# Optimization experiments

Hardware: AMD Instinct MI355X
Metric: run time of the kernel (lower is better)

Reference implementation:

```python
import math
import jax, jax.numpy as jnp
import numpy as np

B, L, D, HID, DFF, EA, NH = 16, 511, 1024, 512, 2048, 256, 4
S = L + 1  # tgt length = bos + L; also memory length (max_basis_dim+1)


def _pe(seq, d):
    pos = jnp.arange(seq, dtype=jnp.float32)[:, None]
    div = jnp.exp(jnp.arange(0, d, 2, dtype=jnp.float32) * (-math.log(10000.0) / d))
    pe = jnp.zeros((seq, d), jnp.float32)
    return pe.at[:, 0::2].set(jnp.sin(pos * div)).at[:, 1::2].set(jnp.cos(pos * div))


def _ln(x, w, b):
    m = x.mean(-1, keepdims=True)
    v = ((x - m) ** 2).mean(-1, keepdims=True)
    return (x - m) / jnp.sqrt(v + 1e-5) * w + b


def _leaky(x):
    return jnp.where(x >= 0, x, 0.01 * x)


def _mha(xq, xkv, qkv_w, qkv_b, out_w, out_b, mask):
    d = xq.shape[-1]
    hd = d // NH
    wq, wk, wv = jnp.split(qkv_w, 3, axis=0)
    bq, bk, bv = jnp.split(qkv_b, 3)
    q = (xq @ wq.T + bq).reshape(xq.shape[0], xq.shape[1], NH, hd)
    k = (xkv @ wk.T + bk).reshape(xkv.shape[0], xkv.shape[1], NH, hd)
    v = (xkv @ wv.T + bv).reshape(xkv.shape[0], xkv.shape[1], NH, hd)
    att = jnp.einsum('bqhd,bkhd->bhqk', q, k) / math.sqrt(hd)
    if mask is not None:
        att = att + mask
    p = jax.nn.softmax(att, axis=-1)
    o = jnp.einsum('bhqk,bkhd->bqhd', p, v).reshape(xq.shape[0], xq.shape[1], d)
    return o @ out_w.T + out_b


def setup_inputs() -> dict:
    key = jax.random.key(0)
    ks = iter(jax.random.split(key, 40))
    rn = lambda shape, s=0.02: jax.random.normal(next(ks), shape, jnp.float32) * s
    return dict(
        gs_norms_embedding=jax.random.normal(next(ks), (B, S, HID), jnp.float32),
        prev_action_embedding=jax.random.normal(next(ks), (B, EA), jnp.float32),
        current_action_embedding=jax.random.normal(next(ks), (B, EA), jnp.float32),
        target_gs_norms=jax.random.normal(next(ks), (B, L), jnp.float32),
        bos=rn((1, 1), 1.0),
        inp_w1=rn((HID, 1)), inp_b1=rn((HID,)),
        inp_w2=rn((HID, HID)), inp_b2=rn((HID,)),
        sa_qkv_w=rn((3, 3 * D, D)), sa_qkv_b=rn((3, 3 * D)),
        sa_out_w=rn((3, D, D)), sa_out_b=rn((3, D)),
        ca_qkv_w=rn((3, 3 * D, D)), ca_qkv_b=rn((3, 3 * D)),
        ca_out_w=rn((3, D, D)), ca_out_b=rn((3, D)),
        ln_w=jnp.ones((3, 3, D), jnp.float32), ln_b=jnp.zeros((3, 3, D), jnp.float32),
        ff_w1=rn((3, DFF, D)), ff_b1=rn((3, DFF)),
        ff_w2=rn((3, D, DFF)), ff_b2=rn((3, D)),
        proj_w1=rn((HID, D)), proj_b1=rn((HID,)),
        proj_w2=rn((1, HID)), proj_b2=rn((1,)),
        basis_dim=jax.random.randint(next(ks), (B,), 0, S),
    )


def reference(gs_norms_embedding, prev_action_embedding, current_action_embedding,
              target_gs_norms, bos, inp_w1, inp_b1, inp_w2, inp_b2,
              sa_qkv_w, sa_qkv_b, sa_out_w, sa_out_b,
              ca_qkv_w, ca_qkv_b, ca_out_w, ca_out_b,
              ln_w, ln_b, ff_w1, ff_b1, ff_w2, ff_b2,
              proj_w1, proj_b1, proj_w2, proj_b2, basis_dim):
    b = gs_norms_embedding.shape[0]
    prev = jnp.broadcast_to(prev_action_embedding[:, None, :], (b, S, EA))
    cur = jnp.broadcast_to(current_action_embedding[:, None, :], (b, S, EA))
    # teacher-forced target: [bos, target] -> input_projection -> pos enc
    tgt_scalar = jnp.concatenate([jnp.broadcast_to(bos, (b, 1)), target_gs_norms], axis=1)  # [B,S]
    x = _leaky(tgt_scalar[..., None] @ inp_w1.T + inp_b1) @ inp_w2.T + inp_b2  # [B,S,HID]
    x = x + _pe(S, HID)
    tgt = jnp.concatenate([x, prev, cur], axis=-1)  # [B,S,D]
    mem = jnp.concatenate([gs_norms_embedding, prev, cur], axis=-1)  # [B,S,D]
    mask = jnp.triu(jnp.full((S, S), -1e9, jnp.float32), k=1)
    h = tgt
    for l in range(3):  # post-norm TransformerDecoderLayer, activation=relu
        h = _ln(h + _mha(h, h, sa_qkv_w[l], sa_qkv_b[l], sa_out_w[l], sa_out_b[l], mask), ln_w[l, 0], ln_b[l, 0])
        h = _ln(h + _mha(h, mem, ca_qkv_w[l], ca_qkv_b[l], ca_out_w[l], ca_out_b[l], None), ln_w[l, 1], ln_b[l, 1])
        ff = jax.nn.relu(h @ ff_w1[l].T + ff_b1[l]) @ ff_w2[l].T + ff_b2[l]
        h = _ln(h + ff, ln_w[l, 2], ln_b[l, 2])
    out = (_leaky(h[:, 1:, :] @ proj_w1.T + proj_b1) @ proj_w2.T + proj_b2)[..., 0]  # [B,L]
    keep = jnp.arange(L)[None, :] < basis_dim[:, None]
    return jnp.where(keep, out, 0.0)
```

## Files before the change

kernel.cpp:

```cpp
#include <hip/hip_runtime.h>

typedef unsigned short u16;
typedef __attribute__((ext_vector_type(8))) short bf16x8;
typedef __attribute__((ext_vector_type(4))) float f32x4;

#define BB   16
#define LL   511
#define SS   512
#define DD   1024
#define HIDD 512
#define DFFF 2048
#define NHH  4
#define HDD  256
#define MTOK (BB*SS)

__device__ __forceinline__ float b2f(u16 u){ return __uint_as_float(((unsigned)u)<<16); }
__device__ __forceinline__ u16 f2b(float f){
    unsigned x = __float_as_uint(f);
    return (u16)((x + 0x7fffu + ((x>>16)&1u)) >> 16);
}
__device__ __forceinline__ float ldin(const void* p, size_t i, int f){
    return f ? ((const float*)p)[i] : b2f(((const u16*)p)[i]);
}
__device__ __forceinline__ void gload_lds16(const void* g, void* l){
    __builtin_amdgcn_global_load_lds((const __attribute__((address_space(1))) unsigned*)g,
                                     (__attribute__((address_space(3))) unsigned*)l, 16, 0, 0);
}

__global__ void detect_kernel(const u16* __restrict__ lnw, int* __restrict__ flag){
    if (threadIdx.x == 0 && blockIdx.x == 0) flag[0] = (lnw[0] == 0x3F80) ? 0 : 1;
}

__global__ void wconv_kernel(const void* __restrict__ w, size_t woff,
                             const void* __restrict__ b, size_t boff,
                             u16* __restrict__ dw, u16* __restrict__ db,
                             int nw, int nb, const int* __restrict__ flag){
    const int f = flag[0];
    const int idx = blockIdx.x*256 + threadIdx.x;
    const int stride = gridDim.x * 256;
    if (f){
        const float* wf = (const float*)w + woff;
        const float* bf = (const float*)b + boff;
        for (int i = idx*4; i < nw; i += stride*4){
            const float4 v = *(const float4*)&wf[i];
            ushort4 o; o.x=f2b(v.x); o.y=f2b(v.y); o.z=f2b(v.z); o.w=f2b(v.w);
            *(ushort4*)&dw[i] = o;
        }
        for (int i = idx*4; i < nb; i += stride*4){
            const float4 v = *(const float4*)&bf[i];
            ushort4 o; o.x=f2b(v.x); o.y=f2b(v.y); o.z=f2b(v.z); o.w=f2b(v.w);
            *(ushort4*)&db[i] = o;
        }
    } else {
        const u16* wu = (const u16*)w + woff;
        const u16* bu = (const u16*)b + boff;
        for (int i = idx*4; i < nw; i += stride*4) *(ushort4*)&dw[i] = *(const ushort4*)&wu[i];
        for (int i = idx*4; i < nb; i += stride*4) *(ushort4*)&db[i] = *(const ushort4*)&bu[i];
    }
}

__global__ void pe_kernel(float* __restrict__ pe){
    const int i = blockIdx.x*256 + threadIdx.x;
    const int s = i >> 9, c = i & 511;
    const float div = expf(-(float)(c & ~1) * (logf(10000.0f)/512.0f));
    const float ang = (float)s * div;
    pe[i] = (c & 1) ? cosf(ang) : sinf(ang);
}

__global__ void inp_u_kernel(const void* __restrict__ bos, const void* __restrict__ target,
                             const void* __restrict__ w1, const void* __restrict__ b1,
                             u16* __restrict__ U, const int* __restrict__ flag){
    const int f = flag[0];
    const int i = blockIdx.x*256 + threadIdx.x;
    const int m = i >> 9, c = i & 511;
    const int b = m >> 9, s = m & 511;
    const float ts = (s == 0) ? ldin(bos, 0, f) : ldin(target, b*LL + s - 1, f);
    float v = ts * ldin(w1, c, f) + ldin(b1, c, f);
    U[i] = f2b(v >= 0.f ? v : 0.01f*v);
}

__global__ void concat_kernel(const void* __restrict__ gs, const void* __restrict__ prev,
                              const void* __restrict__ cur, u16* __restrict__ tgt,
                              u16* __restrict__ mem, const int* __restrict__ flag){
    const int f = flag[0];
    const int i = blockIdx.x*256 + threadIdx.x;
    const int m = i >> 10, c = i & 1023;
    if (c < 512){
        mem[i] = f2b(ldin(gs, (size_t)m*512 + c, f));
    } else {
        const float pc = (c < 768) ? ldin(prev, (m>>9)*256 + (c-512), f)
                                   : ldin(cur,  (m>>9)*256 + (c-768), f);
        const u16 pb = f2b(pc);
        tgt[i] = pb; mem[i] = pb;
    }
}

template<int ACT, int RES>
__device__ __forceinline__ void gemm_body(const u16* __restrict__ A, const u16* __restrict__ W,
                                          const u16* __restrict__ bias, u16* __restrict__ C,
                                          const float* __restrict__ pe, const u16* __restrict__ res,
                                          int K, int ldc){
    __shared__ __align__(16) short As[4096];
    __shared__ __align__(16) short Bs[4096];
    const int m0 = blockIdx.x * 128;
    const int n0 = blockIdx.y * 128;
    const int t  = threadIdx.x;
    const int w = t >> 6, lane = t & 63;
    const int quad = lane >> 4, l16 = lane & 15;
    const int wm = (w >> 1) * 64, wn = (w & 1) * 64;

    f32x4 acc[4][4] = {};

    const u16* Ag = A + (size_t)(m0 + (t>>2))*K + (t&3)*8;
    const u16* Wg = W + (size_t)(n0 + (t>>2))*K + (t&3)*8;
    short* Asd = &As[t*8];
    short* Bsd = &Bs[t*8];
    for (int k0 = 0; k0 < K; k0 += 32){
        __syncthreads();
        gload_lds16(Ag + k0,                 Asd);
        gload_lds16(Ag + (size_t)64*K + k0,  Asd + 2048);
        gload_lds16(Wg + k0,                 Bsd);
        gload_lds16(Wg + (size_t)64*K + k0,  Bsd + 2048);
        __syncthreads();
        bf16x8 af[4], bfr[4];
#pragma unroll
        for (int i=0;i<4;i++) af[i]  = *(const bf16x8*)&As[(wm + i*16 + l16)*32 + quad*8];
#pragma unroll
        for (int j=0;j<4;j++) bfr[j] = *(const bf16x8*)&Bs[(wn + j*16 + l16)*32 + quad*8];
#pragma unroll
        for (int i=0;i<4;i++)
#pragma unroll
            for (int j=0;j<4;j++)
                acc[i][j] = __builtin_amdgcn_mfma_f32_16x16x32_bf16(af[i], bfr[j], acc[i][j], 0,0,0);
    }
#pragma unroll
    for (int i=0;i<4;i++){
        const int rowb = m0 + wm + i*16 + quad*4;
#pragma unroll
        for (int j=0;j<4;j++){
            const int col = n0 + wn + j*16 + l16;
            const float bv = b2f(bias[col]);
#pragma unroll
            for (int r=0;r<4;r++){
                float v = acc[i][j][r] + bv;
                if (pe) v += pe[((rowb + r) & (SS-1))*HIDD + col];
                if (RES) v += b2f(res[(size_t)(rowb + r)*ldc + col]);
                if (ACT == 1) v = fmaxf(v, 0.0f);
                C[(size_t)(rowb + r)*ldc + col] = f2b(v);
            }
        }
    }
}

template<int ACT, int RES>
__global__ __launch_bounds__(256) void gemm_bt(const u16* __restrict__ A, const u16* __restrict__ W,
                                               const u16* __restrict__ bias, u16* __restrict__ C,
                                               const float* __restrict__ pe, const u16* __restrict__ res,
                                               int K, int ldc){
    gemm_body<ACT,RES>(A, W, bias, C, pe, res, K, ldc);
}

__global__ __launch_bounds__(256) void gemm_dual(const u16* __restrict__ A1, const u16* __restrict__ A2,
                                                 const u16* __restrict__ W, const u16* __restrict__ bias,
                                                 u16* __restrict__ C, int K, int ldc){
    const u16* A = (blockIdx.y < 8) ? A1 : A2;
    gemm_body<0,0>(A, W, bias, C, nullptr, nullptr, K, ldc);
}

template<int ACT, int RES, int DUAL>
__global__ __launch_bounds__(512, 2) void gemm_p(const u16* __restrict__ A1, const u16* __restrict__ A2,
                                                 const u16* __restrict__ W, const u16* __restrict__ bias,
                                                 u16* __restrict__ C, const u16* __restrict__ res,
                                                 int K, int ldc){
    __shared__ __align__(16) short lds[36864];
    const int t = threadIdx.x;
    const int w = t >> 6, lane = t & 63;
    const int quad = lane >> 4, l16 = lane & 15;
    const int wm = w >> 2, wn = w & 3;
    const int m0 = blockIdx.x * 128;
    const int n0 = blockIdx.y * 256;
    const u16* A = (DUAL && blockIdx.y >= 4) ? A2 : A1;

    const int srow = t >> 2;
    const int gl   = (t & 3) ^ ((t >> 3) & 3);
    const u16* Ag = A + (size_t)(m0 + srow)*K + gl*8;
    const u16* Bg = W + (size_t)(n0 + srow)*K + gl*8;
    const size_t rstep = (size_t)128 * K;
    short* ldst = &lds[t*8];

    const int koff = (quad ^ ((l16 >> 1) & 3)) * 8;
    const int aoff = (wm*64 + l16)*32 + koff;
    const int boff = 4096 + (wn*64 + l16)*32 + koff;

    f32x4 acc[4][4] = {};
    const int NS = K >> 5;

    gload_lds16(Ag,              ldst);
    gload_lds16(Bg,              ldst + 4096);
    gload_lds16(Bg + rstep,      ldst + 8192);
    gload_lds16(Ag + 32,         ldst + 12288);
    gload_lds16(Bg + 32,         ldst + 12288 + 4096);
    gload_lds16(Bg + rstep + 32, ldst + 12288 + 8192);
    asm volatile("s_waitcnt vmcnt(3)" ::: "memory");
    __builtin_amdgcn_s_barrier();
    asm volatile("" ::: "memory");

    int slot = 0, slot2 = 2;
    for (int s = 0; s < NS; ++s){
        const int sb = slot * 12288;
        const short* Ab = &lds[sb + aoff];
        const short* Bb = &lds[sb + boff];
        bf16x8 av[4], bv[4];
#pragma unroll
        for (int i=0;i<4;i++) av[i] = *(const bf16x8*)(Ab + i*512);
#pragma unroll
        for (int j=0;j<4;j++) bv[j] = *(const bf16x8*)(Bb + j*512);
        const int prefetch = (s + 2 < NS);
        if (prefetch){
            const u16* Ap = Ag + (size_t)(s+2)*32;
            const u16* Bp = Bg + (size_t)(s+2)*32;
            short* ld2 = &lds[slot2*12288 + t*8];
            gload_lds16(Ap,         ld2);
            gload_lds16(Bp,         ld2 + 4096);
            gload_lds16(Bp + rstep, ld2 + 8192);
        }
        asm volatile("s_waitcnt lgkmcnt(0)");
        __builtin_amdgcn_s_setprio(1);
#pragma unroll
        for (int i=0;i<4;i++)
#pragma unroll
            for (int j=0;j<4;j++)
                acc[i][j] = __builtin_amdgcn_mfma_f32_16x16x32_bf16(av[i], bv[j], acc[i][j], 0,0,0);
        __builtin_amdgcn_s_setprio(0);
        if (prefetch) asm volatile("s_waitcnt vmcnt(3)" ::: "memory");
        else          asm volatile("s_waitcnt vmcnt(0)" ::: "memory");
        __builtin_amdgcn_s_barrier();
        asm volatile("" ::: "memory");

        slot  = (slot  == 2) ? 0 : slot  + 1;
        slot2 = (slot2 == 2) ? 0 : slot2 + 1;
    }

#pragma unroll
    for (int i=0;i<4;i++){
        const int rowb = m0 + wm*64 + i*16 + quad*4;
#pragma unroll
        for (int j=0;j<4;j++){
            const int col = n0 + wn*64 + j*16 + l16;
            const float bvv = b2f(bias[col]);
#pragma unroll
            for (int r=0;r<4;r++){
                float v = acc[i][j][r] + bvv;
                if (RES) v += b2f(res[(size_t)(rowb + r)*ldc + col]);
                if (ACT == 1) v = fmaxf(v, 0.0f);
                C[(size_t)(rowb + r)*ldc + col] = f2b(v);
            }
        }
    }
}

__global__ __launch_bounds__(256) void vt_kernel(const u16* __restrict__ qkv, u16* __restrict__ vt){
    __shared__ __align__(16) u16 tile[64][72];
    const int bh = blockIdx.x, b = bh >> 2, h = bh & 3;
    const int s0 = blockIdx.y*64, d0 = blockIdx.z*64;
    const int t = threadIdx.x;
#pragma unroll
    for (int it=0; it<2; it++){
        const int u = it*256 + t;
        const int sl = u >> 3, dc = (u & 7)*8;
        *(uint4*)&tile[sl][dc] =
            *(const uint4*)(qkv + (size_t)(b*SS + s0 + sl)*3072 + 2*DD + h*HDD + d0 + dc);
    }
    __syncthreads();
#pragma unroll
    for (int it=0; it<2; it++){
        const int u = it*256 + t;
        const int dl = u >> 3, sc = (u & 7)*8;
        uint4 tv; u16* tmp = (u16*)&tv;
#pragma unroll
        for (int j=0;j<8;j++) tmp[j] = tile[sc+j][dl];
        *(uint4*)(vt + (size_t)(bh*HDD + d0 + dl)*SS + s0 + sc) = tv;
    }
}

__global__ __launch_bounds__(256) void flash_attn(const u16* __restrict__ qkv, const u16* __restrict__ vt,
                                                  u16* __restrict__ ao, const int causal){
    __shared__ __align__(16) short Kt[2][8192];
    __shared__ __align__(16) short Vs[2][8192];
    __shared__ __align__(16) short pbuf[4][16][40];
    const int bh = blockIdx.x;
    const int qt = causal ? (gridDim.y - 1 - blockIdx.y) : blockIdx.y;
    const int b = bh >> 2, h = bh & 3;
    const int t = threadIdx.x, w = t >> 6, lane = t & 63;
    const int quad = lane >> 4, l16 = lane & 15;
    const int qbase = qt * 64;

    const u16* qp = qkv + (size_t)(b*SS + qbase + w*16 + l16)*3072 + h*HDD + quad*8;
    bf16x8 qf[8];
#pragma unroll
    for (int kc=0;kc<8;kc++) qf[kc] = *(const bf16x8*)(qp + kc*32);

    f32x4 o[16] = {};
    float mrow[4] = {-1e30f,-1e30f,-1e30f,-1e30f};
    float lrow[4] = {0.f,0.f,0.f,0.f};

    const int ntiles = causal ? (qbase/32 + 2) : (SS/32);
    const int myq = qbase + w*16 + quad*4;

    const u16* Kg = qkv + (size_t)(b*SS)*3072 + DD + h*HDD;
    const u16* Vg = vt + (size_t)bh*HDD*SS;
    const int keyl8 = t >> 5;
    const int kslot = t & 31;
    const int vrow4 = t >> 2;
    const int vslot = t & 3;

    auto stage = [&](int kt2, int sl){
        const int kv0s = kt2*32;
#pragma unroll
        for (int j=0;j<4;j++){
            const int keyl = j*8 + keyl8;
            const int ck   = kslot ^ keyl;
            gload_lds16(Kg + (size_t)(kv0s + keyl)*3072 + ck*8, &Kt[sl][j*2048 + t*8]);
            const int d  = j*64 + vrow4;
            const int cv = vslot ^ (d&3) ^ ((d>>2)&3);
            gload_lds16(Vg + (size_t)d*SS + kv0s + cv*8, &Vs[sl][j*2048 + t*8]);
        }
    };

    stage(0, 0);
    for (int kt=0; kt<ntiles; kt++){
        const int kv0 = kt*32;
        const int sl = kt & 1;
        if (kt + 1 < ntiles){
            stage(kt+1, sl^1);
            asm volatile("s_waitcnt vmcnt(8)" ::: "memory");
        } else {
            asm volatile("s_waitcnt vmcnt(0)" ::: "memory");
        }
        __builtin_amdgcn_s_barrier();
        asm volatile("" ::: "memory");

        f32x4 sc0 = {0.f,0.f,0.f,0.f}, sc1 = {0.f,0.f,0.f,0.f};
#pragma unroll
        for (int kk=0;kk<8;kk++){
            const int ch = kk*4 + quad;
            sc0 = __builtin_amdgcn_mfma_f32_16x16x32_bf16(qf[kk],
                    *(const bf16x8*)&Kt[sl][l16*256 + (ch ^ l16)*8], sc0, 0,0,0);
            sc1 = __builtin_amdgcn_mfma_f32_16x16x32_bf16(qf[kk],
                    *(const bf16x8*)&Kt[sl][(16+l16)*256 + (ch ^ (16+l16))*8], sc1, 0,0,0);
        }
#pragma unroll
        for (int r=0;r<4;r++){
            float a0 = sc0[r]*0.0625f, a1 = sc1[r]*0.0625f;
            if (causal){
                if (kv0 + l16 > myq + r)      a0 = -1e9f;
                if (kv0 + 16 + l16 > myq + r) a1 = -1e9f;
            }
            float tm = fmaxf(a0,a1);
            tm = fmaxf(tm, __shfl_xor(tm,1)); tm = fmaxf(tm, __shfl_xor(tm,2));
            tm = fmaxf(tm, __shfl_xor(tm,4)); tm = fmaxf(tm, __shfl_xor(tm,8));
            const float mnew  = fmaxf(mrow[r], tm);
            const float alpha = __expf(mrow[r] - mnew);
            const float p0 = __expf(a0 - mnew), p1 = __expf(a1 - mnew);
            float rs = p0 + p1;
            rs += __shfl_xor(rs,1); rs += __shfl_xor(rs,2);
            rs += __shfl_xor(rs,4); rs += __shfl_xor(rs,8);
            lrow[r] = lrow[r]*alpha + rs;
            mrow[r] = mnew;
#pragma unroll
            for (int dt=0;dt<16;dt++) o[dt][r] *= alpha;
            pbuf[w][quad*4+r][l16]      = (short)f2b(p0);
            pbuf[w][quad*4+r][16 + l16] = (short)f2b(p1);
        }
        asm volatile("s_waitcnt lgkmcnt(0)" ::: "memory");
        __builtin_amdgcn_s_barrier();
        asm volatile("" ::: "memory");

        const bf16x8 pf = *(const bf16x8*)&pbuf[w][l16][quad*8];
#pragma unroll
        for (int dt=0;dt<16;dt++){
            const int d = dt*16 + l16;
            o[dt] = __builtin_amdgcn_mfma_f32_16x16x32_bf16(pf,
                      *(const bf16x8*)&Vs[sl][d*32 + ((quad ^ (d&3) ^ ((d>>2)&3)))*8], o[dt], 0,0,0);
        }
        asm volatile("s_waitcnt lgkmcnt(0)" ::: "memory");
        __builtin_amdgcn_s_barrier();
        asm volatile("" ::: "memory");
    }
#pragma unroll
    for (int r=0;r<4;r++){
        const size_t row = (size_t)(b*SS + myq + r);
        const float inv = 1.0f / lrow[r];
#pragma unroll
        for (int dt=0;dt<16;dt++)
            ao[row*DD + h*HDD + dt*16 + l16] = f2b(o[dt][r]*inv);
    }
}

__global__ __launch_bounds__(256) void ln_kernel(u16* __restrict__ h, const u16* __restrict__ y,
                                                 const void* __restrict__ lnw, const void* __restrict__ lnb,
                                                 size_t off, const int* __restrict__ flag){
    const int f = flag[0];
    const int m = blockIdx.x, t = threadIdx.x;
    __shared__ float red[8];
    const ushort4 yv = *(const ushort4*)&y[(size_t)m*DD + t*4];
    float vv[4]; float sum = 0.f;
    vv[0] = b2f(yv.x); vv[1] = b2f(yv.y); vv[2] = b2f(yv.z); vv[3] = b2f(yv.w);
#pragma unroll
    for (int j=0;j<4;j++) sum += vv[j];
    for (int o2=1; o2<64; o2<<=1) sum += __shfl_xor(sum, o2);
    if ((t&63)==0) red[t>>6] = sum;
    __syncthreads();
    const float mean = (red[0]+red[1]+red[2]+red[3]) * (1.f/DD);
    float vs = 0.f;
#pragma unroll
    for (int j=0;j<4;j++){ const float d = vv[j]-mean; vs += d*d; }
    for (int o2=1; o2<64; o2<<=1) vs += __shfl_xor(vs, o2);
    if ((t&63)==0) red[4 + (t>>6)] = vs;
    __syncthreads();
    const float var = (red[4]+red[5]+red[6]+red[7]) * (1.f/DD);
    const float rstd = rsqrtf(var + 1e-5f);
    ushort4 ov;
    ov.x = f2b((vv[0]-mean)*rstd*ldin(lnw, off+t*4+0, f) + ldin(lnb, off+t*4+0, f));
    ov.y = f2b((vv[1]-mean)*rstd*ldin(lnw, off+t*4+1, f) + ldin(lnb, off+t*4+1, f));
    ov.z = f2b((vv[2]-mean)*rstd*ldin(lnw, off+t*4+2, f) + ldin(lnb, off+t*4+2, f));
    ov.w = f2b((vv[3]-mean)*rstd*ldin(lnw, off+t*4+3, f) + ldin(lnb, off+t*4+3, f));
    *(ushort4*)&h[(size_t)m*DD + t*4] = ov;
}

__global__ __launch_bounds__(256) void final_kernel(const u16* __restrict__ p1, const void* __restrict__ w2,
                                                    const void* __restrict__ b2p, const int* __restrict__ basis,
                                                    void* __restrict__ out, const int* __restrict__ flag){
    const int f = flag[0];
    const int blk = blockIdx.x;
    const int b = blk / LL, l = blk % LL;
    const int t = threadIdx.x;
    __shared__ float red[4];
    const ushort2 pv = *(const ushort2*)&p1[(size_t)(b*SS + l + 1)*HIDD + t*2];
    float acc;
    {
        float v0 = b2f(pv.x); v0 = v0 >= 0.f ? v0 : 0.01f*v0;
        float v1 = b2f(pv.y); v1 = v1 >= 0.f ? v1 : 0.01f*v1;
        acc = v0 * ldin(w2, t*2+0, f) + v1 * ldin(w2, t*2+1, f);
    }
    for (int off=1; off<64; off<<=1) acc += __shfl_xor(acc, off);
    if ((t & 63) == 0) red[t>>6] = acc;
    __syncthreads();
    if (t == 0){
        const float r = red[0]+red[1]+red[2]+red[3] + ldin(b2p, 0, f);
        const float v = (l < basis[b]) ? r : 0.0f;
        if (f) ((float*)out)[blk] = v;
        else   ((u16*)out)[blk] = f2b(v);
    }
}

extern "C" void kernel_launch(void* const* d_in, const int* in_sizes, int n_in,
                              void* d_out, int out_size, void* d_ws, size_t ws_size,
                              hipStream_t stream){
    const void* gs       = d_in[0];
    const void* prev     = d_in[1];
    const void* cur      = d_in[2];
    const void* target   = d_in[3];
    const void* bos      = d_in[4];
    const void* inp_w1   = d_in[5];
    const void* inp_b1   = d_in[6];
    const void* inp_w2   = d_in[7];
    const void* inp_b2   = d_in[8];
    const void* sa_qkv_w = d_in[9];
    const void* sa_qkv_b = d_in[10];
    const void* sa_out_w = d_in[11];
    const void* sa_out_b = d_in[12];
    const void* ca_qkv_w = d_in[13];
    const void* ca_qkv_b = d_in[14];
    const void* ca_out_w = d_in[15];
    const void* ca_out_b = d_in[16];
    const void* ln_w     = d_in[17];
    const void* ln_b     = d_in[18];
    const void* ff_w1    = d_in[19];
    const void* ff_b1    = d_in[20];
    const void* ff_w2    = d_in[21];
    const void* ff_b2    = d_in[22];
    const void* proj_w1  = d_in[23];
    const void* proj_b1  = d_in[24];
    const void* proj_w2  = d_in[25];
    const void* proj_b2  = d_in[26];
    const int*  basis    = (const int*)d_in[27];

    size_t off = 0;
    auto carve = [&](size_t bytes)->void*{
        void* p = (char*)d_ws + off;
        off += (bytes + 255) & ~(size_t)255;
        return p;
    };
    int*   flag = (int*)  carve(256);
    u16*   qkv  = (u16*)  carve((size_t)MTOK*3*DD*2);
    u16*   h    = (u16*)  carve((size_t)MTOK*DD*2);
    u16*   mem  = (u16*)  carve((size_t)MTOK*DD*2);
    u16*   ao   = (u16*)  carve((size_t)MTOK*DD*2);
    u16*   vty  = (u16*)  carve((size_t)MTOK*DD*2);
    float* pe   = (float*)carve((size_t)SS*HIDD*4);
    u16* U  = qkv;
    u16* vt = vty;
    u16* y  = vty;

    const size_t NW_TOTAL = 38535168, NB_TOTAL = 34816;
    const bool full = (ws_size >= off + ((NW_TOTAL*2+255)&~(size_t)255) + ((NB_TOTAL*2+255)&~(size_t)255));

    detect_kernel<<<dim3(1), 64, 0, stream>>>((const u16*)ln_w, flag);
    pe_kernel    <<<dim3(SS*HIDD/256),  256, 0, stream>>>(pe);
    inp_u_kernel <<<dim3(MTOK*HIDD/256),256, 0, stream>>>(bos, target, inp_w1, inp_b1, U, flag);

    if (full){
        u16* wbuf = (u16*)carve(NW_TOTAL*2);
        u16* bbuf = (u16*)carve(NB_TOTAL*2);
        u16* w_saqkv = wbuf + 0;
        u16* w_saout = wbuf + 9437184;
        u16* w_caqkv = wbuf + 12582912;
        u16* w_caout = wbuf + 22020096;
        u16* w_ff1   = wbuf + 25165824;
        u16* w_ff2   = wbuf + 31457280;
        u16* w_inp2  = wbuf + 37748736;
        u16* w_proj1 = wbuf + 38010880;
        u16* b_saqkv = bbuf + 0;
        u16* b_saout = bbuf + 9216;
        u16* b_caqkv = bbuf + 12288;
        u16* b_caout = bbuf + 21504;
        u16* b_ff1   = bbuf + 24576;
        u16* b_ff2   = bbuf + 30720;
        u16* b_inp2  = bbuf + 33792;
        u16* b_proj1 = bbuf + 34304;

        const dim3 wg(1024);
        wconv_kernel<<<wg,256,0,stream>>>(inp_w2,  0, inp_b2,  0, w_inp2,  b_inp2,  HIDD*HIDD, HIDD, flag);
        wconv_kernel<<<wg,256,0,stream>>>(sa_qkv_w,0, sa_qkv_b,0, w_saqkv, b_saqkv, 3*3*DD*DD, 3*3*DD, flag);
        wconv_kernel<<<wg,256,0,stream>>>(sa_out_w,0, sa_out_b,0, w_saout, b_saout, 3*DD*DD,   3*DD,   flag);
        wconv_kernel<<<wg,256,0,stream>>>(ca_qkv_w,0, ca_qkv_b,0, w_caqkv, b_caqkv, 3*3*DD*DD, 3*3*DD, flag);
        wconv_kernel<<<wg,256,0,stream>>>(ca_out_w,0, ca_out_b,0, w_caout, b_caout, 3*DD*DD,   3*DD,   flag);
        wconv_kernel<<<wg,256,0,stream>>>(ff_w1,   0, ff_b1,   0, w_ff1,   b_ff1,   3*DFFF*DD, 3*DFFF, flag);
        wconv_kernel<<<wg,256,0,stream>>>(ff_w2,   0, ff_b2,   0, w_ff2,   b_ff2,   3*DD*DFFF, 3*DD,   flag);
        wconv_kernel<<<wg,256,0,stream>>>(proj_w1, 0, proj_b1, 0, w_proj1, b_proj1, HIDD*DD,   HIDD,   flag);

        gemm_bt<0,0> <<<dim3(64,4),  256, 0, stream>>>(U, w_inp2, b_inp2, h, pe, nullptr, HIDD, DD);
        concat_kernel<<<dim3(MTOK*DD/256), 256, 0, stream>>>(gs, prev, cur, h, mem, flag);

        for (int l = 0; l < 3; l++){
            gemm_p<0,0,0><<<dim3(64,12),512,0,stream>>>(h, nullptr, w_saqkv + (size_t)l*3*DD*DD,
                                                        b_saqkv + l*3*DD, qkv, nullptr, DD, 3*DD);
            vt_kernel    <<<dim3(64,8,4),256,0,stream>>>(qkv, vt);
            flash_attn   <<<dim3(64,8),  256,0,stream>>>(qkv, vt, ao, 1);
            gemm_p<0,1,0><<<dim3(64,4),  512,0,stream>>>(ao, nullptr, w_saout + (size_t)l*DD*DD,
                                                         b_saout + l*DD, y, h, DD, DD);
            ln_kernel    <<<dim3(MTOK),  256,0,stream>>>(h, y, ln_w, ln_b, (size_t)(l*3+0)*DD, flag);

            gemm_p<0,0,1><<<dim3(64,12),512,0,stream>>>(h, mem, w_caqkv + (size_t)l*3*DD*DD,
                                                        b_caqkv + l*3*DD, qkv, nullptr, DD, 3*DD);
            vt_kernel    <<<dim3(64,8,4),256,0,stream>>>(qkv, vt);
            flash_attn   <<<dim3(64,8),  256,0,stream>>>(qkv, vt, ao, 0);
            gemm_p<0,1,0><<<dim3(64,4),  512,0,stream>>>(ao, nullptr, w_caout + (size_t)l*DD*DD,
                                                         b_caout + l*DD, y, h, DD, DD);
            ln_kernel    <<<dim3(MTOK),  256,0,stream>>>(h, y, ln_w, ln_b, (size_t)(l*3+1)*DD, flag);

            gemm_p<1,0,0><<<dim3(64,8), 512,0,stream>>>(h, nullptr, w_ff1 + (size_t)l*DFFF*DD,
                                                        b_ff1 + l*DFFF, qkv, nullptr, DD, DFFF);
            gemm_p<0,1,0><<<dim3(64,4), 512,0,stream>>>(qkv, nullptr, w_ff2 + (size_t)l*DD*DFFF,
                                                        b_ff2 + l*DD, y, h, DFFF, DD);
            ln_kernel    <<<dim3(MTOK), 256,0,stream>>>(h, y, ln_w, ln_b, (size_t)(l*3+2)*DD, flag);
        }
        gemm_bt<0,0><<<dim3(64,4), 256,0,stream>>>(h, w_proj1, b_proj1, y, nullptr, nullptr, DD, HIDD);
        final_kernel<<<dim3(BB*LL),256,0,stream>>>(y, proj_w2, proj_b2, basis, d_out, flag);
    } else {
        u16* s0w = (u16*)carve((size_t)3*DD*DD*2);
        u16* s0b = (u16*)carve((size_t)4096*2);
        u16* s1w = (u16*)carve((size_t)3*DD*DD*2);
        u16* s1b = (u16*)carve((size_t)4096*2);
        const dim3 wcg(512);

        wconv_kernel<<<wcg,256,0,stream>>>(inp_w2, 0, inp_b2, 0, s0w, s0b, HIDD*HIDD, HIDD, flag);
        gemm_bt<0,0><<<dim3(64,4), 256,0,stream>>>(U, s0w, s0b, h, pe, nullptr, HIDD, DD);
        concat_kernel<<<dim3(MTOK*DD/256),256,0,stream>>>(gs, prev, cur, h, mem, flag);

        for (int l = 0; l < 3; l++){
            wconv_kernel<<<wcg,256,0,stream>>>(sa_qkv_w, (size_t)l*3*DD*DD, sa_qkv_b, (size_t)l*3*DD,
                                               s1w, s1b, 3*DD*DD, 3*DD, flag);
            gemm_bt<0,0><<<dim3(64,24),256,0,stream>>>(h, s1w, s1b, qkv, nullptr, nullptr, DD, 3*DD);
            vt_kernel   <<<dim3(64,8,4),256,0,stream>>>(qkv, vt);
            flash_attn  <<<dim3(64,8),  256,0,stream>>>(qkv, vt, ao, 1);
            wconv_kernel<<<wcg,256,0,stream>>>(sa_out_w, (size_t)l*DD*DD, sa_out_b, (size_t)l*DD,
                                               s0w, s0b, DD*DD, DD, flag);
            gemm_bt<0,1><<<dim3(64,8), 256,0,stream>>>(ao, s0w, s0b, y, nullptr, h, DD, DD);
            ln_kernel   <<<dim3(MTOK), 256,0,stream>>>(h, y, ln_w, ln_b, (size_t)(l*3+0)*DD, flag);

            wconv_kernel<<<wcg,256,0,stream>>>(ca_qkv_w, (size_t)l*3*DD*DD, ca_qkv_b, (size_t)l*3*DD,
                                               s1w, s1b, 3*DD*DD, 3*DD, flag);
            gemm_dual   <<<dim3(64,24),256,0,stream>>>(h, mem, s1w, s1b, qkv, DD, 3*DD);
            vt_kernel   <<<dim3(64,8,4),256,0,stream>>>(qkv, vt);
            flash_attn  <<<dim3(64,8),  256,0,stream>>>(qkv, vt, ao, 0);
            wconv_kernel<<<wcg,256,0,stream>>>(ca_out_w, (size_t)l*DD*DD, ca_out_b, (size_t)l*DD,
                                               s0w, s0b, DD*DD, DD, flag);
            gemm_bt<0,1><<<dim3(64,8), 256,0,stream>>>(ao, s0w, s0b, y, nullptr, h, DD, DD);
            ln_kernel   <<<dim3(MTOK), 256,0,stream>>>(h, y, ln_w, ln_b, (size_t)(l*3+1)*DD, flag);

            wconv_kernel<<<wcg,256,0,stream>>>(ff_w1, (size_t)l*DFFF*DD, ff_b1, (size_t)l*DFFF,
                                               s1w, s1b, DFFF*DD, DFFF, flag);
            gemm_bt<1,0><<<dim3(64,16),256,0,stream>>>(h, s1w, s1b, qkv, nullptr, nullptr, DD, DFFF);
            wconv_kernel<<<wcg,256,0,stream>>>(ff_w2, (size_t)l*DD*DFFF, ff_b2, (size_t)l*DD,
                                               s0w, s0b, DD*DFFF, DD, flag);
            gemm_bt<0,1><<<dim3(64,8), 256,0,stream>>>(qkv, s0w, s0b, y, nullptr, h, DFFF, DD);
            ln_kernel   <<<dim3(MTOK), 256,0,stream>>>(h, y, ln_w, ln_b, (size_t)(l*3+2)*DD, flag);
        }
        wconv_kernel<<<wcg,256,0,stream>>>(proj_w1, 0, proj_b1, 0, s1w, s1b, HIDD*DD, HIDD, flag);
        gemm_bt<0,0><<<dim3(64,4), 256,0,stream>>>(h, s1w, s1b, y, nullptr, nullptr, DD, HIDD);
        final_kernel<<<dim3(BB*LL),256,0,stream>>>(y, proj_w2, proj_b2, basis, d_out, flag);
    }
}
```

Baseline: 1.500 ms.

## Deepen gemm_p pipeline to four LDS stages with register double-buffering

Moves the persistent GEMM kernel from a three-slot LDS ring to four slots and unrolls the K loop by two. Fragments for the next step are read from LDS into a second register set while MFMAs run on the current set, which removes the lgkmcnt wait before each MFMA group. LDS per block grows from 72KB to 96KB and register pressure rises with the extra fragment buffers, which may limit occupancy at launch_bounds(512,2). The slot rotation and the vmcnt accounting with three in-flight stages have to stay correct.

```diff
diff --git a/kernel.cpp b/kernel.cpp
--- a/kernel.cpp
+++ b/kernel.cpp
@@ -172,7 +172,7 @@
                                                  const u16* __restrict__ W, const u16* __restrict__ bias,
                                                  u16* __restrict__ C, const u16* __restrict__ res,
                                                  int K, int ldc){
-    __shared__ __align__(16) short lds[36864];
+    __shared__ __align__(16) short lds[49152];
     const int t = threadIdx.x;
     const int w = t >> 6, lane = t & 63;
     const int quad = lane >> 4, l16 = lane & 15;
@@ -195,50 +195,70 @@
     f32x4 acc[4][4] = {};
     const int NS = K >> 5;
 
-    gload_lds16(Ag,              ldst);
-    gload_lds16(Bg,              ldst + 4096);
-    gload_lds16(Bg + rstep,      ldst + 8192);
-    gload_lds16(Ag + 32,         ldst + 12288);
-    gload_lds16(Bg + 32,         ldst + 12288 + 4096);
-    gload_lds16(Bg + rstep + 32, ldst + 12288 + 8192);
+    auto STG = [&](int ss, int sb){
+        const u16* Ap = Ag + (size_t)ss*32;
+        const u16* Bp = Bg + (size_t)ss*32;
+        short* ld2 = ldst + sb;
+        gload_lds16(Ap,         ld2);
+        gload_lds16(Bp,         ld2 + 4096);
+        gload_lds16(Bp + rstep, ld2 + 8192);
+    };
+
+    STG(0, 0); STG(1, 12288); STG(2, 24576);
     asm volatile("s_waitcnt vmcnt(3)" ::: "memory");
     __builtin_amdgcn_s_barrier();
     asm volatile("" ::: "memory");
 
-    int slot = 0, slot2 = 2;
-    for (int s = 0; s < NS; ++s){
-        const int sb = slot * 12288;
-        const short* Ab = &lds[sb + aoff];
-        const short* Bb = &lds[sb + boff];
-        bf16x8 av[4], bv[4];
-#pragma unroll
-        for (int i=0;i<4;i++) av[i] = *(const bf16x8*)(Ab + i*512);
-#pragma unroll
-        for (int j=0;j<4;j++) bv[j] = *(const bf16x8*)(Bb + j*512);
-        const int prefetch = (s + 2 < NS);
-        if (prefetch){
-            const u16* Ap = Ag + (size_t)(s+2)*32;
-            const u16* Bp = Bg + (size_t)(s+2)*32;
-            short* ld2 = &lds[slot2*12288 + t*8];
-            gload_lds16(Ap,         ld2);
-            gload_lds16(Bp,         ld2 + 4096);
-            gload_lds16(Bp + rstep, ld2 + 8192);
-        }
-        asm volatile("s_waitcnt lgkmcnt(0)");
-        __builtin_amdgcn_s_setprio(1);
-#pragma unroll
-        for (int i=0;i<4;i++)
-#pragma unroll
-            for (int j=0;j<4;j++)
-                acc[i][j] = __builtin_amdgcn_mfma_f32_16x16x32_bf16(av[i], bv[j], acc[i][j], 0,0,0);
-        __builtin_amdgcn_s_setprio(0);
-        if (prefetch) asm volatile("s_waitcnt vmcnt(3)" ::: "memory");
-        else          asm volatile("s_waitcnt vmcnt(0)" ::: "memory");
-        __builtin_amdgcn_s_barrier();
-        asm volatile("" ::: "memory");
-
-        slot  = (slot  == 2) ? 0 : slot  + 1;
-        slot2 = (slot2 == 2) ? 0 : slot2 + 1;
+    bf16x8 aE[4], bE[4], aO[4], bO[4];
+#pragma unroll
+    for (int i=0;i<4;i++) aE[i] = *(const bf16x8*)&lds[aoff + i*512];
+#pragma unroll
+    for (int j=0;j<4;j++) bE[j] = *(const bf16x8*)&lds[boff + j*512];
+
+    int sb0 = 0, sb1 = 12288, sb2 = 24576, sb3 = 36864;
+    for (int s = 0; s < NS; s += 2){
+        {
+#pragma unroll
+            for (int i=0;i<4;i++) aO[i] = *(const bf16x8*)&lds[sb1 + aoff + i*512];
+#pragma unroll
+            for (int j=0;j<4;j++) bO[j] = *(const bf16x8*)&lds[sb1 + boff + j*512];
+            const int pf = (s + 3 < NS);
+            if (pf) STG(s+3, sb3);
+            __builtin_amdgcn_s_setprio(1);
+#pragma unroll
+            for (int i=0;i<4;i++)
+#pragma unroll
+                for (int j=0;j<4;j++)
+                    acc[i][j] = __builtin_amdgcn_mfma_f32_16x16x32_bf16(aE[i], bE[j], acc[i][j], 0,0,0);
+            __builtin_amdgcn_s_setprio(0);
+            if (pf) asm volatile("s_waitcnt vmcnt(3)" ::: "memory");
+            else    asm volatile("s_waitcnt vmcnt(0)" ::: "memory");
+            __builtin_amdgcn_s_barrier();
+            asm volatile("" ::: "memory");
+        }
+        {
+            if (s + 2 < NS){
+#pragma unroll
+                for (int i=0;i<4;i++) aE[i] = *(const bf16x8*)&lds[sb2 + aoff + i*512];
+#pragma unroll
+                for (int j=0;j<4;j++) bE[j] = *(const bf16x8*)&lds[sb2 + boff + j*512];
+            }
+            const int pf = (s + 4 < NS);
+            if (pf) STG(s+4, sb0);
+            __builtin_amdgcn_s_setprio(1);
+#pragma unroll
+            for (int i=0;i<4;i++)
+#pragma unroll
+                for (int j=0;j<4;j++)
+                    acc[i][j] = __builtin_amdgcn_mfma_f32_16x16x32_bf16(aO[i], bO[j], acc[i][j], 0,0,0);
+            __builtin_amdgcn_s_setprio(0);
+            if (pf) asm volatile("s_waitcnt vmcnt(3)" ::: "memory");
+            else    asm volatile("s_waitcnt vmcnt(0)" ::: "memory");
+            __builtin_amdgcn_s_barrier();
+            asm volatile("" ::: "memory");
+        }
+        const int x0 = sb0, x1 = sb1;
+        sb0 = sb2; sb1 = sb3; sb2 = x0; sb3 = x1;
     }
 
 #pragma unroll
```

Measured after the change: 1.671 ms. 1.11x slower.
